# Kernel optimization log

Measured on AMD Instinct MI355X. Metric: run time of the kernel, lower is better.

Reference implementation:

```python
import jax, jax.numpy as jnp
import numpy as np

DIM = 256
HEADS = 8
WINDOWS = (1, 2, 4)
B, H, W = 1, 64, 64


def _integral(a):
    # double cumsum over last two dims, then zero-pad one row/col at top/left
    s = jnp.cumsum(jnp.cumsum(a, axis=-2), axis=-1)
    pad = [(0, 0)] * (a.ndim - 2) + [(1, 0), (1, 0)]
    return jnp.pad(s, pad)


def _box(P, ws, Ho, Wo):
    # replicate-pad then box-difference; equivalent to the 2x2 [[1,-1],[-1,1]]
    # kernel conv2d with dilation=ws applied in the torch module.
    tp = ws - 1
    r = tp // 2
    l = tp - r
    pad = [(0, 0)] * (P.ndim - 2) + [(l, r), (l, r)]
    Pp = jnp.pad(P, pad, mode='edge')
    return (Pp[..., ws:ws + Ho, ws:ws + Wo] - Pp[..., ws:ws + Ho, :Wo]
            - Pp[..., :Ho, ws:ws + Wo] + Pp[..., :Ho, :Wo])


def setup_inputs() -> dict:
    key = jax.random.key(0)
    ks = jax.random.split(key, 6)
    x = jax.random.normal(ks[0], (B, DIM, H, W), jnp.float32)
    Wq = jax.random.normal(ks[1], (DIM, DIM), jnp.float32) * 0.05
    Wk = jax.random.normal(ks[2], (DIM, DIM), jnp.float32) * 0.05
    Wv = jax.random.normal(ks[3], (DIM, DIM), jnp.float32) * 0.05
    Wout = jax.random.normal(ks[4], (DIM, DIM * len(WINDOWS)), jnp.float32) * 0.05
    bout = jnp.zeros((DIM,), jnp.float32)
    return {"x": x, "Wq": Wq, "Wk": Wk, "Wv": Wv, "Wout": Wout, "bout": bout}


def reference(x, Wq, Wk, Wv, Wout, bout):
    b, C, Hh, Ww = x.shape
    h = HEADS
    d = C // h
    # 1x1 convs (no bias)
    q = jnp.einsum('bchw,oc->bohw', x, Wq).reshape(b * h, d, Hh, Ww)
    k = jnp.einsum('bchw,oc->bohw', x, Wk).reshape(b * h, d, Hh, Ww)
    v = jnp.einsum('bchw,oc->bohw', x, Wv).reshape(b * h, d, Hh, Ww)
    q = jax.nn.sigmoid(q)
    k = jax.nn.sigmoid(k)
    v = v / jnp.maximum(jnp.linalg.norm(v, axis=1, keepdims=True), 1e-12)

    Ik = _integral(k)                                  # (bh, d, H+1, W+1)
    Ikv = _integral(jnp.einsum('bfhw,bghw->bfghw', k, v))  # (bh, d, d, H+1, W+1)

    outs = []
    for w in WINDOWS:
        ws = Hh // w
        wk = _box(Ik, ws, Hh, Ww)    # (bh, d, H, W)
        wkv = _box(Ikv, ws, Hh, Ww)  # (bh, d, d, H, W)
        attn = jnp.einsum('bdhw,bdfhw->bfhw', q, wkv)
        norm = jnp.einsum('bdhw,bdhw->bhw', q, wk)
        attn = attn / (norm[:, None] + 1e-6)
        outs.append(attn.reshape(b, C, Hh, Ww))
    o = jnp.concatenate(outs, axis=1)  # (b, C*len(WINDOWS), H, W)
    return jnp.einsum('bchw,oc->bohw', o, Wout) + bout[None, :, None, None]
```

## Files before the change

### kernel.cpp

```cpp
#include <hip/hip_runtime.h>
#include <math.h>

#define NPIX 4096
#define CHSZ 3145728
#define NRMSZ 98304

template <int CTRL, int RM>
__device__ __forceinline__ float dpp_add(float x) {
    int xi = __builtin_bit_cast(int, x);
    int sh = __builtin_amdgcn_update_dpp(0, xi, CTRL, RM, 0xf, false);
    return x + __builtin_bit_cast(float, sh);
}

__device__ __forceinline__ float wave_iscan(float x) {
    x = dpp_add<0x111, 0xf>(x);
    x = dpp_add<0x112, 0xf>(x);
    x = dpp_add<0x114, 0xf>(x);
    x = dpp_add<0x118, 0xf>(x);
    x = dpp_add<0x142, 0xa>(x);
    x = dpp_add<0x143, 0xc>(x);
    return x;
}

__device__ __forceinline__ void lds_barrier() {
    asm volatile("s_waitcnt lgkmcnt(0)" ::: "memory");
    __builtin_amdgcn_s_barrier();
    __builtin_amdgcn_sched_barrier(0);
}

__global__ __launch_bounds__(256) void qkv_kernel(
    const float* __restrict__ x, const float* __restrict__ Wq,
    const float* __restrict__ Wk, const float* __restrict__ Wv,
    float* __restrict__ qo, float* __restrict__ ko, float* __restrict__ vo)
{
    const int pt = blockIdx.x * 128;
    const int ot = blockIdx.y * 32;
    const int mat = blockIdx.z;
    const float* __restrict__ W = (mat == 0) ? Wq : ((mat == 1) ? Wk : Wv);
    float* __restrict__ out = (mat == 0) ? qo : ((mat == 1) ? ko : vo);

    __shared__ __align__(16) float Xs[32][132];
    __shared__ __align__(16) float Wt[32][36];

    const int t = threadIdx.x;
    const int pc = t & 31;
    const int oc = t >> 5;
    const int xc = t >> 5;
    const int xp = (t & 31) << 2;
    const int lo = t >> 3;
    const int lg = (t & 7) << 2;

    float4 xf[4];
    float4 wf;
#pragma unroll
    for (int i = 0; i < 4; i++)
        xf[i] = *reinterpret_cast<const float4*>(x + (xc + 8 * i) * NPIX + pt + xp);
    wf = *reinterpret_cast<const float4*>(W + (ot + lo) * 256 + lg);

    float acc[4][4];
#pragma unroll
    for (int j = 0; j < 4; j++)
#pragma unroll
        for (int i = 0; i < 4; i++) acc[j][i] = 0.f;

    for (int kt = 0; kt < 256; kt += 32) {
#pragma unroll
        for (int i = 0; i < 4; i++)
            *reinterpret_cast<float4*>(&Xs[xc + 8 * i][xp]) = xf[i];
        Wt[lg + 0][lo] = wf.x;
        Wt[lg + 1][lo] = wf.y;
        Wt[lg + 2][lo] = wf.z;
        Wt[lg + 3][lo] = wf.w;
        __syncthreads();
        if (kt + 32 < 256) {
#pragma unroll
            for (int i = 0; i < 4; i++)
                xf[i] = *reinterpret_cast<const float4*>(
                    x + (kt + 32 + xc + 8 * i) * NPIX + pt + xp);
            wf = *reinterpret_cast<const float4*>(W + (ot + lo) * 256 + kt + 32 + lg);
        }
#pragma unroll
        for (int kk = 0; kk < 32; kk++) {
            float4 a = *reinterpret_cast<const float4*>(&Xs[kk][pc << 2]);
            float av[4] = {a.x, a.y, a.z, a.w};
            float4 b4 = *reinterpret_cast<const float4*>(&Wt[kk][oc << 2]);
            float bv[4] = {b4.x, b4.y, b4.z, b4.w};
#pragma unroll
            for (int j = 0; j < 4; j++)
#pragma unroll
                for (int i = 0; i < 4; i++)
                    acc[j][i] = fmaf(bv[j], av[i], acc[j][i]);
        }
        __syncthreads();
    }

    if (mat < 2) {
#pragma unroll
        for (int j = 0; j < 4; j++) {
            const int o = ot + (oc << 2) + j;
            float4 r;
            r.x = 1.f / (1.f + __expf(-acc[j][0]));
            r.y = 1.f / (1.f + __expf(-acc[j][1]));
            r.z = 1.f / (1.f + __expf(-acc[j][2]));
            r.w = 1.f / (1.f + __expf(-acc[j][3]));
            *reinterpret_cast<float4*>(out + o * NPIX + pt + (pc << 2)) = r;
        }
    } else {
        float* scratch = &Xs[0][0];
        __syncthreads();
#pragma unroll
        for (int i = 0; i < 4; i++) {
            float ss = 0.f;
#pragma unroll
            for (int j = 0; j < 4; j++) ss += acc[j][i] * acc[j][i];
            scratch[oc * 128 + (pc << 2) + i] = ss;
        }
        __syncthreads();
        float scale[4];
#pragma unroll
        for (int i = 0; i < 4; i++) {
            float tot = 0.f;
#pragma unroll
            for (int g = 0; g < 8; g++) tot += scratch[g * 128 + (pc << 2) + i];
            scale[i] = 1.f / fmaxf(sqrtf(tot), 1e-12f);
        }
#pragma unroll
        for (int j = 0; j < 4; j++) {
            const int o = ot + (oc << 2) + j;
            float4 r;
            r.x = acc[j][0] * scale[0];
            r.y = acc[j][1] * scale[1];
            r.z = acc[j][2] * scale[2];
            r.w = acc[j][3] * scale[3];
            *reinterpret_cast<float4*>(out + o * NPIX + pt + (pc << 2)) = r;
        }
    }
}

template <int PD>
__global__ __launch_bounds__(512) void attn_kernel(
    const float* __restrict__ q, const float* __restrict__ k,
    const float* __restrict__ v, float* __restrict__ num, float* __restrict__ nrm)
{
    const int f = blockIdx.x;
    const int head = blockIdx.y;
    const int dg = blockIdx.z;
    const bool isnorm = (f == 32);

    const float* __restrict__ kh = k + (head * 32 + dg * PD) * NPIX;
    const float* __restrict__ qh = q + (head * 32 + dg * PD) * NPIX;
    const float* __restrict__ vf = v + (head * 32 + (isnorm ? 0 : f)) * NPIX;

    __shared__ __align__(16) float Pt[65][132];
    __shared__ float csum[8][68];

    const int t = threadIdx.x;
    const int lane = t & 63;
    const int wv = t >> 6;

    for (int i = t; i < 65 * 132; i += 512) (&Pt[0][0])[i] = 0.f;

    float vreg[8], kcur[8];
#pragma unroll
    for (int i = 0; i < 8; i++) {
        const int r = wv * 8 + i;
        vreg[i] = isnorm ? 1.f : vf[r * 64 + lane];
        kcur[i] = kh[r * 64 + lane];
    }

    float acc[3][8];
#pragma unroll
    for (int w = 0; w < 3; w++)
#pragma unroll
        for (int i = 0; i < 8; i++) acc[w][i] = 0.f;

    lds_barrier();

    for (int dd = 0; dd < PD; dd++) {
        float qv[8];
#pragma unroll
        for (int g = 0; g < 2; g++)
#pragma unroll
            for (int j = 0; j < 4; j++)
                qv[g * 4 + j] = qh[dd * NPIX + ((wv + 8 * g) * 4 + j) * 64 + lane];

        float pv[8];
        float run = 0.f;
#pragma unroll
        for (int i = 0; i < 8; i++) {
            float rs = wave_iscan(kcur[i] * vreg[i]);
            pv[i] = run;
            run += rs;
        }
        if (dd + 1 < PD) {
#pragma unroll
            for (int i = 0; i < 8; i++)
                kcur[i] = kh[(dd + 1) * NPIX + (wv * 8 + i) * 64 + lane];
        }
        csum[wv][lane] = run;
        lds_barrier();
        float off = 0.f;
#pragma unroll
        for (int w2 = 0; w2 < 7; w2++) if (w2 < wv) off += csum[w2][lane];
#pragma unroll
        for (int i = 0; i < 8; i++) pv[i] += off;
#pragma unroll
        for (int s = 0; s < 2; s++) {
            float4 r4 = make_float4(pv[4 * s], pv[4 * s + 1], pv[4 * s + 2], pv[4 * s + 3]);
            *reinterpret_cast<float4*>(&Pt[lane + 1][32 + wv * 8 + 4 * s]) = r4;
        }
        if (wv == 7) {
            const float tot = off + run;
            const float4 p4 = make_float4(tot, tot, tot, tot);
#pragma unroll
            for (int s = 0; s < 8; s++)
                *reinterpret_cast<float4*>(&Pt[lane + 1][96 + 4 * s]) = p4;
        }
        lds_barrier();
#pragma unroll
        for (int g = 0; g < 2; g++) {
            const int y0 = (wv + 8 * g) * 4;
#pragma unroll
            for (int w = 0; w < 3; w++) {
                const int hw = 32 >> w;
                const int xlo = max(lane - hw, 0);
                const int xhi = min(lane + hw, 64);
                const int ylo = 32 + y0 - hw;
                const int yhi = 32 + y0 + hw;
                float4 A4 = *reinterpret_cast<const float4*>(&Pt[xhi][yhi]);
                float4 B4 = *reinterpret_cast<const float4*>(&Pt[xlo][yhi]);
                float4 C4, E4;
                if (y0 + 3 <= hw) {
                    C4 = make_float4(0.f, 0.f, 0.f, 0.f);
                    E4 = C4;
                } else {
                    C4 = *reinterpret_cast<const float4*>(&Pt[xhi][ylo]);
                    E4 = *reinterpret_cast<const float4*>(&Pt[xlo][ylo]);
                }
                acc[w][g * 4 + 0] = fmaf(qv[g * 4 + 0], (A4.x - B4.x) - (C4.x - E4.x), acc[w][g * 4 + 0]);
                acc[w][g * 4 + 1] = fmaf(qv[g * 4 + 1], (A4.y - B4.y) - (C4.y - E4.y), acc[w][g * 4 + 1]);
                acc[w][g * 4 + 2] = fmaf(qv[g * 4 + 2], (A4.z - B4.z) - (C4.z - E4.z), acc[w][g * 4 + 2]);
                acc[w][g * 4 + 3] = fmaf(qv[g * 4 + 3], (A4.w - B4.w) - (C4.w - E4.w), acc[w][g * 4 + 3]);
            }
        }
    }

    float* __restrict__ nout = num + (size_t)dg * CHSZ;
    float* __restrict__ rout = nrm + (size_t)dg * NRMSZ;
#pragma unroll
    for (int w = 0; w < 3; w++) {
#pragma unroll
        for (int g = 0; g < 2; g++) {
#pragma unroll
            for (int j = 0; j < 4; j++) {
                const int px = ((wv + 8 * g) * 4 + j) * 64 + lane;
                const float val = acc[w][g * 4 + j];
                if (isnorm) rout[(w * 8 + head) * NPIX + px] = val;
                else        nout[((w * 8 + head) * 32 + f) * NPIX + px] = val;
            }
        }
    }
}

template <int NS, int KS>
__global__ __launch_bounds__(256) void out_kernel(
    const float* __restrict__ num, const float* __restrict__ nrm,
    const float* __restrict__ Wout, float* __restrict__ obufA,
    float* __restrict__ obufB)
{
    const int pt = blockIdx.x * 64;
    const int ot = blockIdx.y * 64;
    constexpr int KC = 24 / KS;
    const int kt0 = blockIdx.z * KC;
    __shared__ __align__(16) float As[32][68];
    __shared__ __align__(16) float Wt[32][68];
    const int t = threadIdx.x;
    const int pc = t & 15;
    const int oc = t >> 4;
    const int xc = t >> 4;
    const int xp = (t & 15) << 2;
    const int lo = t & 63;
    const int lc = (t >> 6) << 2;

    float4 nv[NS][2], mv[NS], wf[2];
#pragma unroll
    for (int s = 0; s < NS; s++) {
#pragma unroll
        for (int i = 0; i < 2; i++)
            nv[s][i] = *reinterpret_cast<const float4*>(
                num + (size_t)s * CHSZ + (size_t)(kt0 * 32 + xc + 16 * i) * NPIX + pt + xp);
        mv[s] = *reinterpret_cast<const float4*>(
            nrm + (size_t)s * NRMSZ + kt0 * NPIX + pt + xp);
    }
    wf[0] = *reinterpret_cast<const float4*>(Wout + (ot + lo) * 768 + kt0 * 32 + lc);
    wf[1] = *reinterpret_cast<const float4*>(Wout + (ot + lo) * 768 + kt0 * 32 + lc + 16);

    float acc[4][4];
#pragma unroll
    for (int j = 0; j < 4; j++)
#pragma unroll
        for (int i = 0; i < 4; i++) acc[j][i] = 0.f;

    for (int kt = kt0; kt < kt0 + KC; kt++) {
        float4 ms = mv[0];
#pragma unroll
        for (int s = 1; s < NS; s++) {
            ms.x += mv[s].x; ms.y += mv[s].y; ms.z += mv[s].z; ms.w += mv[s].w;
        }
        float4 rv;
        rv.x = 1.f / (ms.x + 1e-6f); rv.y = 1.f / (ms.y + 1e-6f);
        rv.z = 1.f / (ms.z + 1e-6f); rv.w = 1.f / (ms.w + 1e-6f);
#pragma unroll
        for (int i = 0; i < 2; i++) {
            float4 r = nv[0][i];
#pragma unroll
            for (int s = 1; s < NS; s++) {
                r.x += nv[s][i].x; r.y += nv[s][i].y;
                r.z += nv[s][i].z; r.w += nv[s][i].w;
            }
            r.x *= rv.x; r.y *= rv.y; r.z *= rv.z; r.w *= rv.w;
            *reinterpret_cast<float4*>(&As[xc + 16 * i][xp]) = r;
        }
#pragma unroll
        for (int i = 0; i < 2; i++) {
            Wt[lc + 16 * i + 0][lo] = wf[i].x;
            Wt[lc + 16 * i + 1][lo] = wf[i].y;
            Wt[lc + 16 * i + 2][lo] = wf[i].z;
            Wt[lc + 16 * i + 3][lo] = wf[i].w;
        }
        __syncthreads();
        if (kt + 1 < kt0 + KC) {
#pragma unroll
            for (int s = 0; s < NS; s++) {
#pragma unroll
                for (int i = 0; i < 2; i++)
                    nv[s][i] = *reinterpret_cast<const float4*>(
                        num + (size_t)s * CHSZ +
                        (size_t)((kt + 1) * 32 + xc + 16 * i) * NPIX + pt + xp);
                mv[s] = *reinterpret_cast<const float4*>(
                    nrm + (size_t)s * NRMSZ + (kt + 1) * NPIX + pt + xp);
            }
            wf[0] = *reinterpret_cast<const float4*>(
                Wout + (ot + lo) * 768 + (kt + 1) * 32 + lc);
            wf[1] = *reinterpret_cast<const float4*>(
                Wout + (ot + lo) * 768 + (kt + 1) * 32 + lc + 16);
        }
#pragma unroll
        for (int kk = 0; kk < 32; kk++) {
            float4 a = *reinterpret_cast<const float4*>(&As[kk][pc << 2]);
            float av[4] = {a.x, a.y, a.z, a.w};
            float4 b4 = *reinterpret_cast<const float4*>(&Wt[kk][oc << 2]);
            float bv[4] = {b4.x, b4.y, b4.z, b4.w};
#pragma unroll
            for (int j = 0; j < 4; j++)
#pragma unroll
                for (int i = 0; i < 4; i++)
                    acc[j][i] = fmaf(bv[j], av[i], acc[j][i]);
        }
        __syncthreads();
    }

    float* __restrict__ ob = (KS == 2 || blockIdx.z < 3)
        ? (obufA + (size_t)blockIdx.z * 1048576) : obufB;
#pragma unroll
    for (int j = 0; j < 4; j++) {
        const int o = ot + (oc << 2) + j;
        float4 r;
        r.x = acc[j][0]; r.y = acc[j][1]; r.z = acc[j][2]; r.w = acc[j][3];
        *reinterpret_cast<float4*>(ob + o * NPIX + pt + (pc << 2)) = r;
    }
}

template <int KS>
__global__ __launch_bounds__(256) void kmerge_kernel(
    const float* __restrict__ obufA, const float* __restrict__ obufB,
    const float* __restrict__ bout, float* __restrict__ out)
{
    const int i4 = (blockIdx.x * 256 + threadIdx.x) * 4;
    const float bb = bout[i4 >> 12];
    float4 a = *reinterpret_cast<const float4*>(obufA + i4);
    float4 b = *reinterpret_cast<const float4*>(obufA + 1048576 + i4);
    float rx = a.x + b.x, ry = a.y + b.y, rz = a.z + b.z, rw = a.w + b.w;
    if (KS == 4) {
        float4 c = *reinterpret_cast<const float4*>(obufA + 2097152 + i4);
        float4 d = *reinterpret_cast<const float4*>(obufB + i4);
        rx += c.x + d.x; ry += c.y + d.y; rz += c.z + d.z; rw += c.w + d.w;
    }
    float4 r = make_float4(rx + bb, ry + bb, rz + bb, rw + bb);
    *reinterpret_cast<float4*>(out + i4) = r;
}

extern "C" void kernel_launch(void* const* d_in, const int* in_sizes, int n_in,
                              void* d_out, int out_size, void* d_ws, size_t ws_size,
                              hipStream_t stream)
{
    const float* x    = (const float*)d_in[0];
    const float* Wq   = (const float*)d_in[1];
    const float* Wk   = (const float*)d_in[2];
    const float* Wv   = (const float*)d_in[3];
    const float* Wout = (const float*)d_in[4];
    const float* bout = (const float*)d_in[5];
    float* out = (float*)d_out;

    float* ws = (float*)d_ws;
    float* q   = ws;
    float* k   = ws + 1048576;
    float* v   = ws + 2097152;
    float* num = ws + 3145728;
    float* obufA = ws;
    const size_t fl = ws_size / 4;

    const size_t need_ns4 = 3145728 + (size_t)4 * (CHSZ + NRMSZ);
    const size_t need_ks4 = need_ns4 + 1048576;

    qkv_kernel<<<dim3(32, 8, 3), 256, 0, stream>>>(x, Wq, Wk, Wv, q, k, v);

    if (fl >= need_ks4) {
        float* nrm = num + (size_t)4 * CHSZ;
        float* obufB = ws + need_ns4;
        attn_kernel<8><<<dim3(33, 8, 4), 512, 0, stream>>>(q, k, v, num, nrm);
        out_kernel<4, 4><<<dim3(64, 4, 4), 256, 0, stream>>>(num, nrm, Wout, obufA, obufB);
        kmerge_kernel<4><<<dim3(1024), 256, 0, stream>>>(obufA, obufB, bout, out);
    } else if (fl >= need_ns4) {
        float* nrm = num + (size_t)4 * CHSZ;
        attn_kernel<8><<<dim3(33, 8, 4), 512, 0, stream>>>(q, k, v, num, nrm);
        out_kernel<4, 2><<<dim3(64, 4, 2), 256, 0, stream>>>(num, nrm, Wout, obufA, obufA);
        kmerge_kernel<2><<<dim3(1024), 256, 0, stream>>>(obufA, obufA, bout, out);
    } else if (fl >= 3145728 + (size_t)2 * (CHSZ + NRMSZ)) {
        float* nrm = num + (size_t)2 * CHSZ;
        attn_kernel<16><<<dim3(33, 8, 2), 512, 0, stream>>>(q, k, v, num, nrm);
        out_kernel<2, 2><<<dim3(64, 4, 2), 256, 0, stream>>>(num, nrm, Wout, obufA, obufA);
        kmerge_kernel<2><<<dim3(1024), 256, 0, stream>>>(obufA, obufA, bout, out);
    } else {
        float* nrm = num + CHSZ;
        attn_kernel<32><<<dim3(33, 8, 1), 512, 0, stream>>>(q, k, v, num, nrm);
        out_kernel<1, 2><<<dim3(64, 4, 2), 256, 0, stream>>>(num, nrm, Wout, obufA, obufA);
        kmerge_kernel<2><<<dim3(1024), 256, 0, stream>>>(obufA, obufA, bout, out);
    }
}
```

Measured before the change: 143.4 us.

## Cut attn register pressure and widen out GEMM tile to 128 pixels

```diff
diff --git a/kernel.cpp b/kernel.cpp
--- a/kernel.cpp
+++ b/kernel.cpp
@@ -138,7 +138,7 @@
 }
 
 template <int PD>
-__global__ __launch_bounds__(512) void attn_kernel(
+__global__ __launch_bounds__(512, 4) void attn_kernel(
     const float* __restrict__ q, const float* __restrict__ k,
     const float* __restrict__ v, float* __restrict__ num, float* __restrict__ nrm)
 {
@@ -160,13 +160,10 @@
 
     for (int i = t; i < 65 * 132; i += 512) (&Pt[0][0])[i] = 0.f;
 
-    float vreg[8], kcur[8];
-#pragma unroll
-    for (int i = 0; i < 8; i++) {
-        const int r = wv * 8 + i;
-        vreg[i] = isnorm ? 1.f : vf[r * 64 + lane];
-        kcur[i] = kh[r * 64 + lane];
-    }
+    float vreg[8];
+#pragma unroll
+    for (int i = 0; i < 8; i++)
+        vreg[i] = isnorm ? 1.f : vf[(wv * 8 + i) * 64 + lane];
 
     float acc[3][8];
 #pragma unroll
@@ -177,25 +174,14 @@
     lds_barrier();
 
     for (int dd = 0; dd < PD; dd++) {
-        float qv[8];
-#pragma unroll
-        for (int g = 0; g < 2; g++)
-#pragma unroll
-            for (int j = 0; j < 4; j++)
-                qv[g * 4 + j] = qh[dd * NPIX + ((wv + 8 * g) * 4 + j) * 64 + lane];
-
         float pv[8];
         float run = 0.f;
 #pragma unroll
         for (int i = 0; i < 8; i++) {
-            float rs = wave_iscan(kcur[i] * vreg[i]);
+            const float kv = kh[dd * NPIX + (wv * 8 + i) * 64 + lane];
+            float rs = wave_iscan(kv * vreg[i]);
             pv[i] = run;
             run += rs;
-        }
-        if (dd + 1 < PD) {
-#pragma unroll
-            for (int i = 0; i < 8; i++)
-                kcur[i] = kh[(dd + 1) * NPIX + (wv * 8 + i) * 64 + lane];
         }
         csum[wv][lane] = run;
         lds_barrier();
@@ -220,6 +206,10 @@
 #pragma unroll
         for (int g = 0; g < 2; g++) {
             const int y0 = (wv + 8 * g) * 4;
+            float qv[4];
+#pragma unroll
+            for (int j = 0; j < 4; j++)
+                qv[j] = qh[dd * NPIX + (y0 + j) * 64 + lane];
 #pragma unroll
             for (int w = 0; w < 3; w++) {
                 const int hw = 32 >> w;
@@ -237,10 +227,10 @@
                     C4 = *reinterpret_cast<const float4*>(&Pt[xhi][ylo]);
                     E4 = *reinterpret_cast<const float4*>(&Pt[xlo][ylo]);
                 }
-                acc[w][g * 4 + 0] = fmaf(qv[g * 4 + 0], (A4.x - B4.x) - (C4.x - E4.x), acc[w][g * 4 + 0]);
-                acc[w][g * 4 + 1] = fmaf(qv[g * 4 + 1], (A4.y - B4.y) - (C4.y - E4.y), acc[w][g * 4 + 1]);
-                acc[w][g * 4 + 2] = fmaf(qv[g * 4 + 2], (A4.z - B4.z) - (C4.z - E4.z), acc[w][g * 4 + 2]);
-                acc[w][g * 4 + 3] = fmaf(qv[g * 4 + 3], (A4.w - B4.w) - (C4.w - E4.w), acc[w][g * 4 + 3]);
+                acc[w][g * 4 + 0] = fmaf(qv[0], (A4.x - B4.x) - (C4.x - E4.x), acc[w][g * 4 + 0]);
+                acc[w][g * 4 + 1] = fmaf(qv[1], (A4.y - B4.y) - (C4.y - E4.y), acc[w][g * 4 + 1]);
+                acc[w][g * 4 + 2] = fmaf(qv[2], (A4.z - B4.z) - (C4.z - E4.z), acc[w][g * 4 + 2]);
+                acc[w][g * 4 + 3] = fmaf(qv[3], (A4.w - B4.w) - (C4.w - E4.w), acc[w][g * 4 + 3]);
             }
         }
     }
@@ -263,15 +253,134 @@
 }
 
 template <int NS, int KS>
-__global__ __launch_bounds__(256) void out_kernel(
+__global__ __launch_bounds__(256) void out128_kernel(
     const float* __restrict__ num, const float* __restrict__ nrm,
     const float* __restrict__ Wout, float* __restrict__ obufA,
     float* __restrict__ obufB)
 {
-    const int pt = blockIdx.x * 64;
+    const int pt = blockIdx.x * 128;
     const int ot = blockIdx.y * 64;
     constexpr int KC = 24 / KS;
     const int kt0 = blockIdx.z * KC;
+    __shared__ __align__(16) float As[32][132];
+    __shared__ __align__(16) float Wt[32][68];
+    const int t = threadIdx.x;
+    const int pc = t & 31;
+    const int oc = t >> 5;
+    const int xc = t >> 5;
+    const int xp = (t & 31) << 2;
+    const int lo = t & 63;
+    const int lc = (t >> 6) << 2;
+
+    float4 snv[4], smv, wf[2];
+#pragma unroll
+    for (int i = 0; i < 4; i++) {
+        snv[i] = *reinterpret_cast<const float4*>(
+            num + (size_t)(kt0 * 32 + xc + 8 * i) * NPIX + pt + xp);
+#pragma unroll
+        for (int s = 1; s < NS; s++) {
+            float4 v2 = *reinterpret_cast<const float4*>(
+                num + (size_t)s * CHSZ + (size_t)(kt0 * 32 + xc + 8 * i) * NPIX + pt + xp);
+            snv[i].x += v2.x; snv[i].y += v2.y; snv[i].z += v2.z; snv[i].w += v2.w;
+        }
+    }
+    smv = *reinterpret_cast<const float4*>(nrm + kt0 * NPIX + pt + xp);
+#pragma unroll
+    for (int s = 1; s < NS; s++) {
+        float4 v2 = *reinterpret_cast<const float4*>(
+            nrm + (size_t)s * NRMSZ + kt0 * NPIX + pt + xp);
+        smv.x += v2.x; smv.y += v2.y; smv.z += v2.z; smv.w += v2.w;
+    }
+    wf[0] = *reinterpret_cast<const float4*>(Wout + (ot + lo) * 768 + kt0 * 32 + lc);
+    wf[1] = *reinterpret_cast<const float4*>(Wout + (ot + lo) * 768 + kt0 * 32 + lc + 16);
+
+    float acc[8][4];
+#pragma unroll
+    for (int j = 0; j < 8; j++)
+#pragma unroll
+        for (int i = 0; i < 4; i++) acc[j][i] = 0.f;
+
+    for (int kt = kt0; kt < kt0 + KC; kt++) {
+        float4 rv;
+        rv.x = 1.f / (smv.x + 1e-6f); rv.y = 1.f / (smv.y + 1e-6f);
+        rv.z = 1.f / (smv.z + 1e-6f); rv.w = 1.f / (smv.w + 1e-6f);
+#pragma unroll
+        for (int i = 0; i < 4; i++) {
+            float4 r;
+            r.x = snv[i].x * rv.x; r.y = snv[i].y * rv.y;
+            r.z = snv[i].z * rv.z; r.w = snv[i].w * rv.w;
+            *reinterpret_cast<float4*>(&As[xc + 8 * i][xp]) = r;
+        }
+#pragma unroll
+        for (int i = 0; i < 2; i++) {
+            Wt[lc + 16 * i + 0][lo] = wf[i].x;
+            Wt[lc + 16 * i + 1][lo] = wf[i].y;
+            Wt[lc + 16 * i + 2][lo] = wf[i].z;
+            Wt[lc + 16 * i + 3][lo] = wf[i].w;
+        }
+        __syncthreads();
+        if (kt + 1 < kt0 + KC) {
+#pragma unroll
+            for (int i = 0; i < 4; i++) {
+                snv[i] = *reinterpret_cast<const float4*>(
+                    num + (size_t)((kt + 1) * 32 + xc + 8 * i) * NPIX + pt + xp);
+#pragma unroll
+                for (int s = 1; s < NS; s++) {
+                    float4 v2 = *reinterpret_cast<const float4*>(
+                        num + (size_t)s * CHSZ +
+                        (size_t)((kt + 1) * 32 + xc + 8 * i) * NPIX + pt + xp);
+                    snv[i].x += v2.x; snv[i].y += v2.y;
+                    snv[i].z += v2.z; snv[i].w += v2.w;
+                }
+            }
+            smv = *reinterpret_cast<const float4*>(
+                nrm + (kt + 1) * NPIX + pt + xp);
+#pragma unroll
+            for (int s = 1; s < NS; s++) {
+                float4 v2 = *reinterpret_cast<const float4*>(
+                    nrm + (size_t)s * NRMSZ + (kt + 1) * NPIX + pt + xp);
+                smv.x += v2.x; smv.y += v2.y; smv.z += v2.z; smv.w += v2.w;
+            }
+            wf[0] = *reinterpret_cast<const float4*>(
+                Wout + (ot + lo) * 768 + (kt + 1) * 32 + lc);
+            wf[1] = *reinterpret_cast<const float4*>(
+                Wout + (ot + lo) * 768 + (kt + 1) * 32 + lc + 16);
+        }
+#pragma unroll
+        for (int kk = 0; kk < 32; kk++) {
+            float4 a = *reinterpret_cast<const float4*>(&As[kk][pc << 2]);
+            float av[4] = {a.x, a.y, a.z, a.w};
+            float4 b0 = *reinterpret_cast<const float4*>(&Wt[kk][oc << 3]);
+            float4 b1 = *reinterpret_cast<const float4*>(&Wt[kk][(oc << 3) + 4]);
+            float bv[8] = {b0.x, b0.y, b0.z, b0.w, b1.x, b1.y, b1.z, b1.w};
+#pragma unroll
+            for (int j = 0; j < 8; j++)
+#pragma unroll
+                for (int i = 0; i < 4; i++)
+                    acc[j][i] = fmaf(bv[j], av[i], acc[j][i]);
+        }
+        __syncthreads();
+    }
+
+    float* __restrict__ ob = (blockIdx.z < 3)
+        ? (obufA + (size_t)blockIdx.z * 1048576) : obufB;
+#pragma unroll
+    for (int j = 0; j < 8; j++) {
+        const int o = ot + (oc << 3) + j;
+        float4 r;
+        r.x = acc[j][0]; r.y = acc[j][1]; r.z = acc[j][2]; r.w = acc[j][3];
+        *reinterpret_cast<float4*>(ob + o * NPIX + pt + (pc << 2)) = r;
+    }
+}
+
+template <int NS>
+__global__ __launch_bounds__(256) void out64_kernel(
+    const float* __restrict__ num, const float* __restrict__ nrm,
+    const float* __restrict__ Wout, float* __restrict__ obuf)
+{
+    const int pt = blockIdx.x * 64;
+    const int ot = blockIdx.y * 64;
+    const int kt0 = blockIdx.z * 12;
     __shared__ __align__(16) float As[32][68];
     __shared__ __align__(16) float Wt[32][68];
     const int t = threadIdx.x;
@@ -301,7 +410,7 @@
 #pragma unroll
         for (int i = 0; i < 4; i++) acc[j][i] = 0.f;
 
-    for (int kt = kt0; kt < kt0 + KC; kt++) {
+    for (int kt = kt0; kt < kt0 + 12; kt++) {
         float4 ms = mv[0];
 #pragma unroll
         for (int s = 1; s < NS; s++) {
@@ -329,7 +438,7 @@
             Wt[lc + 16 * i + 3][lo] = wf[i].w;
         }
         __syncthreads();
-        if (kt + 1 < kt0 + KC) {
+        if (kt + 1 < kt0 + 12) {
 #pragma unroll
             for (int s = 0; s < NS; s++) {
 #pragma unroll
@@ -360,8 +469,7 @@
         __syncthreads();
     }
 
-    float* __restrict__ ob = (KS == 2 || blockIdx.z < 3)
-        ? (obufA + (size_t)blockIdx.z * 1048576) : obufB;
+    float* __restrict__ ob = obuf + (size_t)blockIdx.z * 1048576;
 #pragma unroll
     for (int j = 0; j < 4; j++) {
         const int o = ot + (oc << 2) + j;
@@ -419,22 +527,22 @@
         float* nrm = num + (size_t)4 * CHSZ;
         float* obufB = ws + need_ns4;
         attn_kernel<8><<<dim3(33, 8, 4), 512, 0, stream>>>(q, k, v, num, nrm);
-        out_kernel<4, 4><<<dim3(64, 4, 4), 256, 0, stream>>>(num, nrm, Wout, obufA, obufB);
+        out128_kernel<4, 4><<<dim3(32, 4, 4), 256, 0, stream>>>(num, nrm, Wout, obufA, obufB);
         kmerge_kernel<4><<<dim3(1024), 256, 0, stream>>>(obufA, obufB, bout, out);
     } else if (fl >= need_ns4) {
         float* nrm = num + (size_t)4 * CHSZ;
         attn_kernel<8><<<dim3(33, 8, 4), 512, 0, stream>>>(q, k, v, num, nrm);
-        out_kernel<4, 2><<<dim3(64, 4, 2), 256, 0, stream>>>(num, nrm, Wout, obufA, obufA);
+        out64_kernel<4><<<dim3(64, 4, 2), 256, 0, stream>>>(num, nrm, Wout, obufA);
         kmerge_kernel<2><<<dim3(1024), 256, 0, stream>>>(obufA, obufA, bout, out);
     } else if (fl >= 3145728 + (size_t)2 * (CHSZ + NRMSZ)) {
         float* nrm = num + (size_t)2 * CHSZ;
         attn_kernel<16><<<dim3(33, 8, 2), 512, 0, stream>>>(q, k, v, num, nrm);
-        out_kernel<2, 2><<<dim3(64, 4, 2), 256, 0, stream>>>(num, nrm, Wout, obufA, obufA);
+        out64_kernel<2><<<dim3(64, 4, 2), 256, 0, stream>>>(num, nrm, Wout, obufA);
         kmerge_kernel<2><<<dim3(1024), 256, 0, stream>>>(obufA, obufA, bout, out);
     } else {
         float* nrm = num + CHSZ;
         attn_kernel<32><<<dim3(33, 8, 1), 512, 0, stream>>>(q, k, v, num, nrm);
-        out_kernel<1, 2><<<dim3(64, 4, 2), 256, 0, stream>>>(num, nrm, Wout, obufA, obufA);
+        out64_kernel<1><<<dim3(64, 4, 2), 256, 0, stream>>>(num, nrm, Wout, obufA);
         kmerge_kernel<2><<<dim3(1024), 256, 0, stream>>>(obufA, obufA, bout, out);
     }
 }
```

Result: faster. 124.0 us (-13.5%).
